# Kernel optimization log

Measured on AMD Instinct MI355X. Metric: run time of the kernel, lower is better.

Reference implementation:

```python
import jax, jax.numpy as jnp
import numpy as np

B, L, E, C = 256, 1024, 128, 5  # trees, leaves per tree, embed size, num classes

def setup_inputs() -> dict:
    key = jax.random.key(0)
    k1, k2, k3 = jax.random.split(key, 3)
    leaves = jax.random.normal(k1, (B, L, E), dtype=jnp.float32)
    # Glorot-ish scaling so 10 stacked relu(Linear) levels stay well-conditioned
    W = jax.random.normal(k2, (E, 2 * E), dtype=jnp.float32) * (2.0 / (2 * E)) ** 0.5
    bW = jnp.zeros((E,), dtype=jnp.float32)
    P = jax.random.normal(k3, (C, E), dtype=jnp.float32) * (2.0 / E) ** 0.5
    bP = jnp.zeros((C,), dtype=jnp.float32)
    return {"leaves": leaves, "W": W, "bW": bW, "P": P, "bP": bP}

def reference(leaves, W, bW, P, bP):
    """Batched level-by-level bottom-up pass over a forest of perfect binary trees.
    Per internal node (same math as RecursiveNN.traverse):
        h = relu(W @ concat(left, right) + bW)
        proj = P @ h + bP
    Returns all internal-node projections concatenated: [B*(L-1), C].
    """
    x = leaves  # [B, n, E] current frontier of node embeddings
    probs = []
    while x.shape[1] > 1:
        # pair adjacent siblings: [B, n/2, 2E]
        pairs = jnp.concatenate([x[:, 0::2], x[:, 1::2]], axis=-1)
        h = jax.nn.relu(jnp.einsum('bnf,ef->bne', pairs, W) + bW)  # [B, n/2, E]
        proj = jnp.einsum('bne,ce->bnc', h, P) + bP                # [B, n/2, C]
        probs.append(proj.reshape(-1, P.shape[0]))
        x = h
    return jnp.concatenate(probs, axis=0)  # [B*(L-1), C]
```

## Files before the change

### kernel.cpp

```cpp
#include <hip/hip_runtime.h>
#include <hip/hip_bf16.h>
#include <hip/hip_fp16.h>


typedef _Float16 f16_t;
typedef _Float16 f16x4 __attribute__((ext_vector_type(4)));
typedef _Float16 f16x8 __attribute__((ext_vector_type(8)));
typedef float f32x4 __attribute__((ext_vector_type(4)));

#define HSTRIDE 136

static __device__ __forceinline__ f32x4 mfma16(f16x8 a, f16x8 b, f32x4 c) {
    return __builtin_amdgcn_mfma_f32_16x16x32_f16(a, b, c, 0, 0, 0);
}

__global__ void prep_kernel(const float* __restrict__ W, const float* __restrict__ P,
                            f16_t* __restrict__ Wh, f16_t* __restrict__ Ph) {
    if (blockIdx.x < 128) {
        const int i = blockIdx.x * 256 + threadIdx.x;
        Wh[i] = (f16_t)W[i];
    } else {
        for (int i = threadIdx.x; i < 640; i += 256) Ph[i] = (f16_t)P[i];
    }
}

__global__ __launch_bounds__(256, 2)
void forest_kernel(const float* __restrict__ leaves,
                   const f16_t* __restrict__ Wh,
                   const f16_t* __restrict__ Ph,
                   const float* __restrict__ bW,
                   const float* __restrict__ bP,
                   f16_t* __restrict__ Q,
                   float* __restrict__ out)
{
    __shared__ f16_t Arena[128 * HSTRIDE];
    __shared__ f16_t Hbuf[64 * HSTRIDE];
    __shared__ float OutB[320];

    const int tid   = threadIdx.x;
    const int wave  = tid >> 6;
    const int lane  = tid & 63;
    const int mlane = lane & 15;
    const int q     = lane >> 4;
    const int tree  = blockIdx.x >> 3;
    const int e     = blockIdx.x & 7;
    const size_t m0 = (size_t)blockIdx.x * 64;
    const float* leafbase = leaves + (size_t)blockIdx.x * 16384;

    f16x8 wh[2][8];
    float bwv[2];
    #pragma unroll
    for (int n = 0; n < 2; ++n) {
        const int col = wave * 32 + n * 16 + mlane;
        bwv[n] = bW[col];
        #pragma unroll
        for (int k = 0; k < 8; ++k)
            wh[n][k] = *(const f16x8*)&Wh[col * 256 + k * 32 + q * 8];
    }

    f16x8 pb[4] = {};
    if (mlane < 5) {
        #pragma unroll
        for (int kb = 0; kb < 4; ++kb)
            pb[kb] = *(const f16x8*)&Ph[mlane * 128 + kb * 32 + q * 8];
    }
    const float bpv = (mlane < 5) ? bP[mlane] : 0.f;

    #pragma unroll
    for (int b = 0; b < 2; ++b) {
        float4 t[8];
        #pragma unroll
        for (int r = 0; r < 8; ++r)
            t[r] = ((const float4*)leafbase)[tid + (b * 8 + r) * 256];
        #pragma unroll
        for (int r = 0; r < 8; ++r) {
            const int idx = tid + (b * 8 + r) * 256;
            const int row = idx >> 5;
            const int c4  = idx & 31;
            f16x4 t4 = { (f16_t)t[r].x, (f16_t)t[r].y, (f16_t)t[r].z, (f16_t)t[r].w };
            *(f16x4*)&Arena[row * HSTRIDE + c4 * 4] = t4;
        }
    }
    __syncthreads();

    #pragma unroll
    for (int c = 0; c < 4; ++c) {
        f16x8 af[8];
        #pragma unroll
        for (int k = 0; k < 8; ++k) {
            const int off  = k * 64 + q * 16;
            const int trow = off >> 8;
            const int ce   = (off & 255) >> 1;
            af[k] = *(const f16x8*)&Arena[(32 * c + 2 * mlane + trow) * HSTRIDE + ce];
        }
        f32x4 acc0 = {}, acc1 = {};
        #pragma unroll
        for (int k = 0; k < 8; ++k) {
            acc0 = mfma16(af[k], wh[0][k], acc0);
            acc1 = mfma16(af[k], wh[1][k], acc1);
        }
        #pragma unroll
        for (int r = 0; r < 4; ++r) {
            float v0 = fmaxf(acc0[r] + bwv[0], 0.f);
            float v1 = fmaxf(acc1[r] + bwv[1], 0.f);
            Hbuf[(c * 16 + q * 4 + r) * HSTRIDE + wave * 32 + mlane]      = (f16_t)v0;
            Hbuf[(c * 16 + q * 4 + r) * HSTRIDE + wave * 32 + 16 + mlane] = (f16_t)v1;
        }
    }
    __syncthreads();

    {
        const int hrow0 = wave * 16;
        f32x4 pc = {};
        #pragma unroll
        for (int kb = 0; kb < 4; ++kb) {
            const f16x8 ha = *(const f16x8*)&Hbuf[(hrow0 + mlane) * HSTRIDE + kb * 32 + q * 8];
            pc = mfma16(ha, pb[kb], pc);
        }
        if (mlane < 5) {
            #pragma unroll
            for (int r = 0; r < 4; ++r) {
                const int row = q * 4 + r;
                out[(m0 + hrow0 + row) * 5 + mlane] = pc[r] + bpv;
            }
        }
    }

    int Mprev = 64;
    #pragma unroll 1
    for (int j = 2; j <= 7; ++j) {
        const int Mnew   = Mprev >> 1;
        const int chunks = (Mnew + 15) >> 4;
        const int obase  = 64 - (256 >> j);
        for (int c = 0; c < chunks; ++c) {
            f16x8 af[8];
            #pragma unroll
            for (int k = 0; k < 8; ++k) {
                const int off  = k * 64 + q * 16;
                const int trow = off >> 8;
                const int ce   = (off & 255) >> 1;
                af[k] = *(const f16x8*)&Hbuf[(32 * c + 2 * mlane + trow) * HSTRIDE + ce];
            }
            __syncthreads();
            f32x4 acc0 = {}, acc1 = {};
            #pragma unroll
            for (int k = 0; k < 8; ++k) {
                acc0 = mfma16(af[k], wh[0][k], acc0);
                acc1 = mfma16(af[k], wh[1][k], acc1);
            }
            #pragma unroll
            for (int r = 0; r < 4; ++r) {
                float v0 = fmaxf(acc0[r] + bwv[0], 0.f);
                float v1 = fmaxf(acc1[r] + bwv[1], 0.f);
                Hbuf[(c * 16 + q * 4 + r) * HSTRIDE + wave * 32 + mlane]      = (f16_t)v0;
                Hbuf[(c * 16 + q * 4 + r) * HSTRIDE + wave * 32 + 16 + mlane] = (f16_t)v1;
            }
            __syncthreads();

            const int valid = (Mnew - c * 16 < 16) ? (Mnew - c * 16) : 16;
            if (wave == 0) {
                f32x4 pc = {};
                #pragma unroll
                for (int kb = 0; kb < 4; ++kb) {
                    const f16x8 ha = *(const f16x8*)&Hbuf[(c * 16 + mlane) * HSTRIDE + kb * 32 + q * 8];
                    pc = mfma16(ha, pb[kb], pc);
                }
                if (mlane < 5) {
                    #pragma unroll
                    for (int r = 0; r < 4; ++r) {
                        const int row = q * 4 + r;
                        if (row < valid)
                            OutB[(obase + c * 16 + row) * 5 + mlane] = pc[r] + bpv;
                    }
                }
            }
        }
        Mprev = Mnew;
    }
    __syncthreads();

    for (int t2 = tid; t2 < 315; t2 += 256) {
        const int lrow = t2 / 5;
        const int cls  = t2 - lrow * 5;
        int j, i;
        if      (lrow < 32) { j = 2; i = lrow;      }
        else if (lrow < 48) { j = 3; i = lrow - 32; }
        else if (lrow < 56) { j = 4; i = lrow - 48; }
        else if (lrow < 60) { j = 5; i = lrow - 56; }
        else if (lrow < 62) { j = 6; i = lrow - 60; }
        else                { j = 7; i = 0;         }
        const size_t grow = (size_t)256 * (1024 - (2048 >> j))
                          + (size_t)tree * (1024 >> j) + (size_t)e * (128 >> j) + i;
        out[grow * 5 + cls] = OutB[t2];
    }

    if (tid < 16)
        *(uint4*)&Q[(size_t)blockIdx.x * 128 + tid * 8] = *(const uint4*)&Hbuf[tid * 8];
}

__global__ __launch_bounds__(128, 4)
void rnn_top_kernel(const f16_t* __restrict__ Q,
                    const float* __restrict__ W,
                    const float* __restrict__ bW,
                    const float* __restrict__ P,
                    const float* __restrict__ bP,
                    float* __restrict__ out)
{
    __shared__ float qs[1024];
    __shared__ float hs[896];
    const int t    = threadIdx.x;
    const int tree = blockIdx.x;

    #pragma unroll
    for (int i = 0; i < 8; ++i)
        qs[t + i * 128] = (float)Q[(size_t)tree * 1024 + t + i * 128];
    __syncthreads();

    const float* wr = W + t * 256;

    float s8[4];
    #pragma unroll
    for (int n = 0; n < 4; ++n) s8[n] = bW[t];
    for (int k = 0; k < 256; k += 4) {
        const float4 wv = *(const float4*)(wr + k);
        #pragma unroll
        for (int n = 0; n < 4; ++n) {
            const float* qb = qs + n * 256 + k;
            s8[n] += wv.x * qb[0] + wv.y * qb[1] + wv.z * qb[2] + wv.w * qb[3];
        }
    }
    #pragma unroll
    for (int n = 0; n < 4; ++n) hs[n * 128 + t] = fmaxf(s8[n], 0.f);
    __syncthreads();

    float s9[2];
    s9[0] = s9[1] = bW[t];
    for (int k = 0; k < 256; k += 4) {
        const float4 wv = *(const float4*)(wr + k);
        #pragma unroll
        for (int m = 0; m < 2; ++m) {
            const float* hb = hs + m * 256 + k;
            s9[m] += wv.x * hb[0] + wv.y * hb[1] + wv.z * hb[2] + wv.w * hb[3];
        }
    }
    hs[512 + t] = fmaxf(s9[0], 0.f);
    hs[640 + t] = fmaxf(s9[1], 0.f);
    __syncthreads();

    float s10 = bW[t];
    for (int k = 0; k < 256; k += 4) {
        const float4 wv = *(const float4*)(wr + k);
        const float* hb = hs + 512 + k;
        s10 += wv.x * hb[0] + wv.y * hb[1] + wv.z * hb[2] + wv.w * hb[3];
    }
    hs[768 + t] = fmaxf(s10, 0.f);
    __syncthreads();

    if (t < 35) {
        const int node = t / 5, c = t % 5;
        float s = bP[c];
        const float* hb = hs + node * 128;
        for (int k = 0; k < 128; ++k) s += hb[k] * P[c * 128 + k];
        size_t row;
        if (node < 4)      row = 260096 + (size_t)tree * 4 + node;
        else if (node < 6) row = 261120 + (size_t)tree * 2 + (node - 4);
        else               row = 261632 + (size_t)tree;
        out[row * 5 + c] = s;
    }
}

extern "C" void kernel_launch(void* const* d_in, const int* in_sizes, int n_in,
                              void* d_out, int out_size, void* d_ws, size_t ws_size,
                              hipStream_t stream) {
    const float* leaves = (const float*)d_in[0];
    const float* W      = (const float*)d_in[1];
    const float* bW     = (const float*)d_in[2];
    const float* P      = (const float*)d_in[3];
    const float* bP     = (const float*)d_in[4];
    float* out = (float*)d_out;

    f16_t* Wh = (f16_t*)d_ws;
    f16_t* Ph = Wh + 32768;
    f16_t* Q  = Wh + 32768 + 1024;

    prep_kernel<<<dim3(129), dim3(256), 0, stream>>>(W, P, Wh, Ph);
    forest_kernel<<<dim3(2048), dim3(256), 0, stream>>>(leaves, Wh, Ph, bW, bP, Q, out);
    rnn_top_kernel<<<dim3(256), dim3(128), 0, stream>>>(Q, W, bW, P, bP, out);
}
```

Baseline: 226.6 us.

## Unroll level schedule with in-place LDS ping-pong and spread projections across waves

Replaces the per-chunk level loop, which had two barriers per chunk, with a fully unrolled schedule. Each level step writes into a separate region of one LDS arena, so the read barrier before each write is no longer needed. Small-level projections are now spread across different waves instead of always running on wave 0. Level-1 projections are staged through a larger OutB buffer and written out together with the other levels instead of being stored directly. LDS use drops from a 64-row to a 32-row second buffer, which could improve occupancy, at the cost of more intricate manual buffer aliasing that must stay race-free.

```diff
diff --git a/kernel.cpp b/kernel.cpp
--- a/kernel.cpp
+++ b/kernel.cpp
@@ -33,9 +33,9 @@
                    f16_t* __restrict__ Q,
                    float* __restrict__ out)
 {
-    __shared__ f16_t Arena[128 * HSTRIDE];
-    __shared__ f16_t Hbuf[64 * HSTRIDE];
-    __shared__ float OutB[320];
+    __shared__ f16_t AR[128 * HSTRIDE];
+    __shared__ f16_t HB2[32 * HSTRIDE];
+    __shared__ float OutB[640];
 
     const int tid   = threadIdx.x;
     const int wave  = tid >> 6;
@@ -44,7 +44,6 @@
     const int q     = lane >> 4;
     const int tree  = blockIdx.x >> 3;
     const int e     = blockIdx.x & 7;
-    const size_t m0 = (size_t)blockIdx.x * 64;
     const float* leafbase = leaves + (size_t)blockIdx.x * 16384;
 
     f16x8 wh[2][8];
@@ -78,20 +77,18 @@
             const int row = idx >> 5;
             const int c4  = idx & 31;
             f16x4 t4 = { (f16_t)t[r].x, (f16_t)t[r].y, (f16_t)t[r].z, (f16_t)t[r].w };
-            *(f16x4*)&Arena[row * HSTRIDE + c4 * 4] = t4;
-        }
-    }
-    __syncthreads();
-
-    #pragma unroll
-    for (int c = 0; c < 4; ++c) {
+            *(f16x4*)&AR[row * HSTRIDE + c4 * 4] = t4;
+        }
+    }
+
+    auto level_step = [&](const f16_t* src, f16_t* dst) {
         f16x8 af[8];
         #pragma unroll
         for (int k = 0; k < 8; ++k) {
             const int off  = k * 64 + q * 16;
             const int trow = off >> 8;
             const int ce   = (off & 255) >> 1;
-            af[k] = *(const f16x8*)&Arena[(32 * c + 2 * mlane + trow) * HSTRIDE + ce];
+            af[k] = *(const f16x8*)&src[(2 * mlane + trow) * HSTRIDE + ce];
         }
         f32x4 acc0 = {}, acc1 = {};
         #pragma unroll
@@ -103,99 +100,87 @@
         for (int r = 0; r < 4; ++r) {
             float v0 = fmaxf(acc0[r] + bwv[0], 0.f);
             float v1 = fmaxf(acc1[r] + bwv[1], 0.f);
-            Hbuf[(c * 16 + q * 4 + r) * HSTRIDE + wave * 32 + mlane]      = (f16_t)v0;
-            Hbuf[(c * 16 + q * 4 + r) * HSTRIDE + wave * 32 + 16 + mlane] = (f16_t)v1;
-        }
-    }
-    __syncthreads();
-
-    {
-        const int hrow0 = wave * 16;
+            dst[(q * 4 + r) * HSTRIDE + wave * 32 + mlane]      = (f16_t)v0;
+            dst[(q * 4 + r) * HSTRIDE + wave * 32 + 16 + mlane] = (f16_t)v1;
+        }
+    };
+
+    auto proj_to_outb = [&](const f16_t* hb, int orow0, int valid) {
         f32x4 pc = {};
         #pragma unroll
         for (int kb = 0; kb < 4; ++kb) {
-            const f16x8 ha = *(const f16x8*)&Hbuf[(hrow0 + mlane) * HSTRIDE + kb * 32 + q * 8];
+            const f16x8 ha = *(const f16x8*)&hb[mlane * HSTRIDE + kb * 32 + q * 8];
             pc = mfma16(ha, pb[kb], pc);
         }
         if (mlane < 5) {
             #pragma unroll
             for (int r = 0; r < 4; ++r) {
                 const int row = q * 4 + r;
-                out[(m0 + hrow0 + row) * 5 + mlane] = pc[r] + bpv;
+                if (row < valid) OutB[(orow0 + row) * 5 + mlane] = pc[r] + bpv;
             }
         }
-    }
-
-    int Mprev = 64;
-    #pragma unroll 1
-    for (int j = 2; j <= 7; ++j) {
-        const int Mnew   = Mprev >> 1;
-        const int chunks = (Mnew + 15) >> 4;
-        const int obase  = 64 - (256 >> j);
-        for (int c = 0; c < chunks; ++c) {
-            f16x8 af[8];
-            #pragma unroll
-            for (int k = 0; k < 8; ++k) {
-                const int off  = k * 64 + q * 16;
-                const int trow = off >> 8;
-                const int ce   = (off & 255) >> 1;
-                af[k] = *(const f16x8*)&Hbuf[(32 * c + 2 * mlane + trow) * HSTRIDE + ce];
-            }
-            __syncthreads();
-            f32x4 acc0 = {}, acc1 = {};
-            #pragma unroll
-            for (int k = 0; k < 8; ++k) {
-                acc0 = mfma16(af[k], wh[0][k], acc0);
-                acc1 = mfma16(af[k], wh[1][k], acc1);
-            }
-            #pragma unroll
-            for (int r = 0; r < 4; ++r) {
-                float v0 = fmaxf(acc0[r] + bwv[0], 0.f);
-                float v1 = fmaxf(acc1[r] + bwv[1], 0.f);
-                Hbuf[(c * 16 + q * 4 + r) * HSTRIDE + wave * 32 + mlane]      = (f16_t)v0;
-                Hbuf[(c * 16 + q * 4 + r) * HSTRIDE + wave * 32 + 16 + mlane] = (f16_t)v1;
-            }
-            __syncthreads();
-
-            const int valid = (Mnew - c * 16 < 16) ? (Mnew - c * 16) : 16;
-            if (wave == 0) {
-                f32x4 pc = {};
-                #pragma unroll
-                for (int kb = 0; kb < 4; ++kb) {
-                    const f16x8 ha = *(const f16x8*)&Hbuf[(c * 16 + mlane) * HSTRIDE + kb * 32 + q * 8];
-                    pc = mfma16(ha, pb[kb], pc);
-                }
-                if (mlane < 5) {
-                    #pragma unroll
-                    for (int r = 0; r < 4; ++r) {
-                        const int row = q * 4 + r;
-                        if (row < valid)
-                            OutB[(obase + c * 16 + row) * 5 + mlane] = pc[r] + bpv;
-                    }
-                }
-            }
-        }
-        Mprev = Mnew;
-    }
-    __syncthreads();
-
-    for (int t2 = tid; t2 < 315; t2 += 256) {
+    };
+
+    __syncthreads();
+
+    level_step(&AR[ 0 * HSTRIDE], &HB2[ 0 * HSTRIDE]);
+    level_step(&AR[32 * HSTRIDE], &HB2[16 * HSTRIDE]);
+    __syncthreads();
+    level_step(&AR[64 * HSTRIDE], &AR[ 0 * HSTRIDE]);
+    level_step(&AR[96 * HSTRIDE], &AR[16 * HSTRIDE]);
+    __syncthreads();
+
+    {
+        const f16_t* pbase = (wave < 2) ? &HB2[(wave * 16) * HSTRIDE]
+                                        : &AR[((wave - 2) * 16) * HSTRIDE];
+        proj_to_outb(pbase, wave * 16, 16);
+    }
+
+    level_step(&HB2[0 * HSTRIDE], &AR[32 * HSTRIDE]);
+    level_step(&AR [0 * HSTRIDE], &AR[48 * HSTRIDE]);
+    __syncthreads();
+    if (wave == 0) proj_to_outb(&AR[32 * HSTRIDE], 64, 16);
+    if (wave == 1) proj_to_outb(&AR[48 * HSTRIDE], 80, 16);
+
+    level_step(&AR[32 * HSTRIDE], &AR[0 * HSTRIDE]);
+    __syncthreads();
+    if (wave == 2) proj_to_outb(&AR[0 * HSTRIDE], 96, 16);
+
+    level_step(&AR[0 * HSTRIDE], &AR[16 * HSTRIDE]);
+    __syncthreads();
+    if (wave == 3) proj_to_outb(&AR[16 * HSTRIDE], 112, 8);
+
+    level_step(&AR[16 * HSTRIDE], &AR[24 * HSTRIDE]);
+    __syncthreads();
+    if (wave == 0) proj_to_outb(&AR[24 * HSTRIDE], 120, 4);
+
+    level_step(&AR[24 * HSTRIDE], &AR[28 * HSTRIDE]);
+    __syncthreads();
+    if (wave == 1) proj_to_outb(&AR[28 * HSTRIDE], 124, 2);
+
+    level_step(&AR[28 * HSTRIDE], &AR[30 * HSTRIDE]);
+    __syncthreads();
+    if (wave == 2) proj_to_outb(&AR[30 * HSTRIDE], 126, 1);
+    __syncthreads();
+
+    for (int t2 = tid; t2 < 635; t2 += 256) {
         const int lrow = t2 / 5;
         const int cls  = t2 - lrow * 5;
         int j, i;
-        if      (lrow < 32) { j = 2; i = lrow;      }
-        else if (lrow < 48) { j = 3; i = lrow - 32; }
-        else if (lrow < 56) { j = 4; i = lrow - 48; }
-        else if (lrow < 60) { j = 5; i = lrow - 56; }
-        else if (lrow < 62) { j = 6; i = lrow - 60; }
-        else                { j = 7; i = 0;         }
+        if      (lrow <  64) { j = 1; i = lrow;       }
+        else if (lrow <  96) { j = 2; i = lrow - 64;  }
+        else if (lrow < 112) { j = 3; i = lrow - 96;  }
+        else if (lrow < 120) { j = 4; i = lrow - 112; }
+        else if (lrow < 124) { j = 5; i = lrow - 120; }
+        else if (lrow < 126) { j = 6; i = lrow - 124; }
+        else                 { j = 7; i = 0;          }
         const size_t grow = (size_t)256 * (1024 - (2048 >> j))
                           + (size_t)tree * (1024 >> j) + (size_t)e * (128 >> j) + i;
         out[grow * 5 + cls] = OutB[t2];
     }
 
     if (tid < 16)
-        *(uint4*)&Q[(size_t)blockIdx.x * 128 + tid * 8] = *(const uint4*)&Hbuf[tid * 8];
+        *(uint4*)&Q[(size_t)blockIdx.x * 128 + tid * 8] = *(const uint4*)&AR[30 * HSTRIDE + tid * 8];
 }
 
 __global__ __launch_bounds__(128, 4)
```

Result: no change. 225.2 us (-0.6%).
